# Kernel tuning notes

Measured on AMD Instinct MI355X. Metric: run time of the kernel, lower is better.

## Reference

```python
import jax, jax.numpy as jnp
import numpy as np

EPS = 1e-6
SCALE = 1.0
GRID_HEIGHT = 4.0
GRID_RES_Y = 1.0


def _perspective(mat, vec):
    # mat [3,4], vec [...,3] -> (points [...,2], flag [...,3])
    homog = jnp.einsum('ij,...j->...i', mat[:, :3], vec) + mat[:, 3]
    pos = homog[..., 2:3] > 0
    flag = jnp.concatenate([pos, pos, jnp.ones_like(pos)], axis=-1).astype(homog.dtype)
    homog = homog * flag  # zero x,y behind camera; z kept (flag[...,-1]=True)
    return homog[..., :2] / homog[..., 2:3], flag


def _fisheye(pts, k, D, flag):
    cx, cy, fx, fy = k[0, 2], k[1, 2], k[0, 0], k[1, 1]
    x = (pts[..., 0] - cx) / fx
    y = (pts[..., 1] - cy) / fy
    r = jnp.sqrt(x * x + y * y)
    th = jnp.arctan(r)
    t2 = th * th
    rad = th * (1 + D[0] * t2 + D[1] * t2 ** 2 + D[2] * t2 ** 3 + D[5] * t2 ** 4) / r
    xd = x * rad * fx + cx
    yd = y * rad * fy + cy
    return jnp.stack([xd, yd], axis=-1) * flag[..., :2]


def _pinhole(pts, k, D, flag):
    cx, cy, fx, fy = k[0, 2], k[1, 2], k[0, 0], k[1, 1]
    x = (pts[..., 0] - cx) / fx
    y = (pts[..., 1] - cy) / fy
    k1, k2, k3, p1, p2 = D[0], D[1], D[2], D[3], D[4]
    r2 = x * x + y * y
    poly = 1 + k1 * r2 + k2 * r2 * r2 + k3 * r2 * r2 * r2
    xd = x * poly + (2 * p1 * x * y + p2 * (r2 + 2 * x * x))
    yd = y * poly + (p1 * (r2 + 2 * y * y) + 2 * p2 * x * y)
    return jnp.stack([xd * fx + cx, yd * fy + cy], axis=-1) * flag[..., :2]


def _bilinear(img, coords):
    # torch F.grid_sample(align_corners=True, padding_mode='border'); img [C,H,W], coords [...,2] in [-1,1]
    C, H, W = img.shape
    x = jnp.clip((coords[..., 0] + 1) * 0.5 * (W - 1), 0.0, W - 1)
    y = jnp.clip((coords[..., 1] + 1) * 0.5 * (H - 1), 0.0, H - 1)
    x0 = jnp.floor(x)
    y0 = jnp.floor(y)
    wx = x - x0
    wy = y - y0
    x0i = x0.astype(jnp.int32)
    y0i = y0.astype(jnp.int32)
    x1i = jnp.minimum(x0i + 1, W - 1)
    y1i = jnp.minimum(y0i + 1, H - 1)
    flat = img.reshape(C, H * W)

    def g(yi, xi):
        return jnp.take(flat, (yi * W + xi).reshape(-1), axis=1).reshape((C,) + coords.shape[:-1])

    v00 = g(y0i, x0i)
    v01 = g(y0i, x1i)
    v10 = g(y1i, x0i)
    v11 = g(y1i, x1i)
    return v00 * (1 - wx) * (1 - wy) + v01 * wx * (1 - wy) + v10 * (1 - wx) * wy + v11 * wx * wy


def _per_image(feature, k, imu2c, post_rot, post_tran, undist, corner):
    C, Hf, Wf = feature.shape
    calib = k @ imu2c                                  # [3,4]
    pts, flag = _perspective(calib, corner)            # pts [Ny,Zd,Xd,2]
    pts = jnp.where(undist[-1] == 1,
                    _fisheye(pts, k, undist, flag),
                    _pinhole(pts, k, undist, flag))
    pts = jnp.einsum('ij,...j->...i', post_rot[:2, :2], pts) + post_tran[:2]
    nc = jnp.clip(2.0 * (pts / SCALE) - 1.0, -1.0, 1.0)  # [Ny,Zd,Xd,2]
    s0, s1 = slice(None, -1), slice(1, None)
    # 8 voxel corners -> [8, Ny-1, D, Wd, 2]
    corners8 = jnp.stack([nc[a, b, c] for a in (s0, s1) for b in (s0, s1) for c in (s0, s1)], axis=0)
    left = corners8[..., 0].min(0)
    right = corners8[..., 0].max(0)
    top = corners8[..., 1].min(0)
    bot = corners8[..., 1].max(0)
    Nh, D, Wd = left.shape
    bbox = jnp.stack([left, top, right, bot], axis=-1).reshape(Nh, D * Wd, 4)
    area = (bbox[..., 2] - bbox[..., 0]) * (bbox[..., 3] - bbox[..., 1]) * Hf * Wf * 0.25 + EPS  # [Nh,P]
    integ = jnp.cumsum(jnp.cumsum(feature, axis=-1), axis=-2)  # integral image [C,Hf,Wf]
    tl = _bilinear(integ, bbox[..., 0:2])
    br = _bilinear(integ, bbox[..., 2:4])
    tr = _bilinear(integ, jnp.stack([bbox[..., 2], bbox[..., 1]], axis=-1))
    bl = _bilinear(integ, jnp.stack([bbox[..., 0], bbox[..., 3]], axis=-1))
    vox = (tl + br - tr - bl) / area * (area > EPS)    # [C,Nh,P]
    return vox.reshape(C * Nh, D, Wd)                  # neck == '2d'


def _forward(features, ks, imu2cs, post_rots, post_trans, undists, grid):
    ys = -jnp.arange(0.0, GRID_HEIGHT, GRID_RES_Y) + GRID_HEIGHT / 2.0
    y_corners = jnp.stack([jnp.zeros_like(ys), ys, jnp.zeros_like(ys)], axis=-1)  # [Ny,3]
    corners = grid[:, None] + y_corners[None, :, None, None, :]                   # [B,Ny,Zd,Xd,3]
    per_cam = jax.vmap(_per_image, in_axes=(0, 0, 0, 0, 0, 0, None))

    def per_batch(f, k, m, pr, pt, ud, c):
        # drop_idx = [] -> all cameras kept; max over cameras
        return per_cam(f, k, m, pr, pt, ud, c).max(axis=0)

    return jax.vmap(per_batch)(features, ks, imu2cs, post_rots, post_trans, undists, corners)


def setup_inputs():
    key = jax.random.key(0)
    B, N, C, Hf, Wf = 1, 6, 64, 64, 176
    Zd = Xd = 129
    kf, ku = jax.random.split(key, 2)
    features = jax.random.normal(kf, (B, N, C, Hf, Wf), jnp.float32)
    # intrinsics (realistic pinhole values keep the projection numerically sane)
    K = np.zeros((B, N, 3, 3), np.float32)
    K[..., 0, 0] = 600.0
    K[..., 1, 1] = 600.0
    K[..., 0, 2] = 704.0
    K[..., 1, 2] = 256.0
    K[..., 2, 2] = 1.0
    ks = jnp.asarray(K)
    # extrinsics: per-camera yaw + small translation
    m = np.zeros((B, N, 3, 4), np.float32)
    for i in range(N):
        th = 0.25 * (i - 2.5)
        R = np.array([[np.cos(th), 0.0, np.sin(th)],
                      [0.0, 1.0, 0.0],
                      [-np.sin(th), 0.0, np.cos(th)]], np.float32)
        m[:, i, :, :3] = R
        m[:, i, :, 3] = np.array([0.1 * i, -1.5, 0.2], np.float32)
    imu2cs = jnp.asarray(m)
    pr = np.zeros((B, N, 3, 3), np.float32)
    pr[..., 0, 0] = 1.0 / 1408.0
    pr[..., 1, 1] = 1.0 / 512.0
    pr[..., 2, 2] = 1.0
    post_rots = jnp.asarray(pr)
    post_trans = jnp.zeros((B, N, 3), jnp.float32)
    und = 0.01 * np.array(jax.random.normal(ku, (B, N, 7)), np.float32)
    und[..., 6] = 0.0
    und[:, :3, 6] = 1.0  # first 3 cameras fisheye, rest pinhole
    undists = jnp.asarray(und)
    x = np.linspace(-40.0, 40.0, Xd, dtype=np.float32)
    z = np.linspace(3.0, 80.0, Zd, dtype=np.float32)
    zz, xx = np.meshgrid(z, x, indexing='ij')
    g = np.stack([xx, np.zeros_like(xx), zz], axis=-1)[None]  # [1,Zd,Xd,3]
    grid = jnp.asarray(np.broadcast_to(g, (B, Zd, Xd, 3)).copy())
    return {"features": features, "ks": ks, "imu2cs": imu2cs, "post_rots": post_rots,
            "post_trans": post_trans, "undists": undists, "grid": grid}


def reference(features, ks, imu2cs, post_rots, post_trans, undists, grid):
    return _forward(features, ks, imu2cs, post_rots, post_trans, undists, grid)
```

## Files before the change

### kernel.cpp

```cpp
#include <hip/hip_runtime.h>
#include <math.h>

#define NCAM 6
#define C_CH 64
#define HF   64
#define WF   176
#define GDIM 129
#define NY   4
#define NH   3
#define DD   128
#define WDIM 128
#define NP   (DD*WDIM)

#define ROWB (WF*C_CH*4)
#define COLB (C_CH*4)
#define IMGB ((size_t)HF*WF*C_CH*4)

struct alignas(16) BoxP {
    int   r0, r1, r2, r3;
    int   c0, c1, c2, c3;
    float wxL, wxR, wyT, wyB;
    float area;
    int   pad0, pad1, pad2;
};
static_assert(sizeof(BoxP) == 64, "BoxP size");

__device__ __forceinline__ int rfl_i(int x) {
    return __builtin_amdgcn_readfirstlane(x);
}
__device__ __forceinline__ float rfl_f(float x) {
    return __builtin_bit_cast(float, __builtin_amdgcn_readfirstlane(__builtin_bit_cast(int, x)));
}

__global__ __launch_bounds__(256) void k_rowcum(const float* __restrict__ feat,
                                                float* __restrict__ rowsum)
{
    __shared__ float T[WF * 65];
    __shared__ float S[4][C_CH];
    __shared__ float OFF[4][C_CH];
    const int h   = blockIdx.x;
    const int n   = blockIdx.y;
    const int tid = threadIdx.x;

    for (int idx = tid; idx < C_CH * WF; idx += 256) {
        const int cc = idx / WF;
        const int w  = idx % WF;
        T[w*65 + cc] = feat[((size_t)(n*C_CH + cc)*HF + h)*WF + w];
    }
    __syncthreads();
    {
        const int cc = tid & 63, seg = tid >> 6;
        const int w0 = seg * 44;
        float run = 0.0f;
        #pragma unroll
        for (int i = 0; i < 44; ++i) {
            run += T[(w0 + i)*65 + cc];
            T[(w0 + i)*65 + cc] = run;
        }
        S[seg][cc] = run;
    }
    __syncthreads();
    {
        const int cc = tid & 63, seg = tid >> 6;
        float off = 0.0f;
        #pragma unroll
        for (int s = 0; s < 3; ++s)
            if (s < seg) off += S[s][cc];
        OFF[seg][cc] = off;
    }
    __syncthreads();
    float* outp = rowsum + (size_t)(n*HF + h) * (WF * C_CH);
    for (int idx = tid; idx < WF * C_CH; idx += 256) {
        const int w  = idx >> 6;
        const int cc = idx & 63;
        outp[idx] = T[w*65 + cc] + OFF[w/44][cc];
    }
}

__global__ __launch_bounds__(256) void k_colcum(const float* __restrict__ rowsum,
                                                float* __restrict__ integ)
{
    __shared__ float tA[4][C_CH];
    const int x  = blockIdx.x;
    const int n  = blockIdx.y;
    const int c  = threadIdx.x & 63;
    const int hq = threadIdx.x >> 6;

    const float* base = rowsum + (size_t)n*HF*WF*C_CH + (size_t)x * C_CH + c;
    float e[16];
    #pragma unroll
    for (int i = 0; i < 16; ++i)
        e[i] = base[(size_t)(hq*16 + i) * (WF*C_CH)];
    #pragma unroll
    for (int i = 1; i < 16; ++i)
        e[i] += e[i-1];
    tA[hq][c] = e[15];
    __syncthreads();
    float off = 0.0f;
    #pragma unroll
    for (int s = 0; s < 3; ++s)
        if (s < hq) off += tA[s][c];
    float* outp = integ + (size_t)n*HF*WF*C_CH + (size_t)x * C_CH + c;
    #pragma unroll
    for (int i = 0; i < 16; ++i)
        outp[(size_t)(hq*16 + i) * (WF*C_CH)] = e[i] + off;
}

__global__ void k_boxproj(const float* __restrict__ ks,
                          const float* __restrict__ imu2cs,
                          const float* __restrict__ post_rots,
                          const float* __restrict__ post_trans,
                          const float* __restrict__ undists,
                          const float* __restrict__ grid,
                          BoxP* __restrict__ bp)
{
    const int idx = blockIdx.x * blockDim.x + threadIdx.x;
    if (idx >= NCAM * NH * NP) return;
    const int n  = idx / (NH * NP);
    const int r  = idx % (NH * NP);
    const int nh = r / NP;
    const int p  = r % NP;
    const int d  = p / WDIM;
    const int wd = p % WDIM;

    const float* k  = ks         + n * 9;
    const float* m  = imu2cs     + n * 12;
    const float* pr = post_rots  + n * 9;
    const float* pt = post_trans + n * 3;
    const float* D  = undists    + n * 7;

    float cal[12];
    #pragma unroll
    for (int i = 0; i < 3; ++i)
        #pragma unroll
        for (int j = 0; j < 4; ++j)
            cal[i*4+j] = k[i*3+0]*m[0*4+j] + k[i*3+1]*m[1*4+j] + k[i*3+2]*m[2*4+j];

    const float fx = k[0], fy = k[4], cx = k[2], cy = k[5];
    const bool fish = (D[6] == 1.0f);
    const float D0 = D[0], D1 = D[1], D2 = D[2], D3 = D[3], D4 = D[4], D5 = D[5];

    float left = 1e30f, right = -1e30f, top = 1e30f, bot = -1e30f;
    #pragma unroll
    for (int a = 0; a < 2; ++a) {
        const float vy = 2.0f - (float)(nh + a);
        #pragma unroll
        for (int b = 0; b < 2; ++b) {
            #pragma unroll
            for (int cc = 0; cc < 2; ++cc) {
                const int gz = d + b, gx = wd + cc;
                const float vx = grid[(gz*GDIM + gx)*3 + 0];
                const float vz = grid[(gz*GDIM + gx)*3 + 2];

                const float hx = cal[0]*vx + cal[1]*vy + cal[2]*vz  + cal[3];
                const float hy = cal[4]*vx + cal[5]*vy + cal[6]*vz  + cal[7];
                const float hz = cal[8]*vx + cal[9]*vy + cal[10]*vz + cal[11];

                const float fl = (hz > 0.0f) ? 1.0f : 0.0f;
                const float px = (hx * fl) / hz;
                const float py = (hy * fl) / hz;

                const float x = (px - cx) / fx;
                const float y = (py - cy) / fy;

                float xd, yd;
                if (fish) {
                    const float rr = sqrtf(x*x + y*y);
                    const float th = atanf(rr);
                    const float t2 = th * th;
                    const float t4 = t2 * t2;
                    const float rad = th * (1.0f + D0*t2 + D1*t4 + D2*(t2*t4) + D5*(t4*t4)) / rr;
                    xd = x * rad * fx + cx;
                    yd = y * rad * fy + cy;
                } else {
                    const float r2 = x*x + y*y;
                    const float poly = 1.0f + D0*r2 + D1*r2*r2 + D2*r2*r2*r2;
                    const float xdd = x*poly + (2.0f*D3*x*y + D4*(r2 + 2.0f*x*x));
                    const float ydd = y*poly + (D3*(r2 + 2.0f*y*y) + 2.0f*D4*x*y);
                    xd = xdd * fx + cx;
                    yd = ydd * fy + cy;
                }
                xd *= fl; yd *= fl;

                const float qx = pr[0]*xd + pr[1]*yd + pt[0];
                const float qy = pr[3]*xd + pr[4]*yd + pt[1];
                const float ncx = fminf(fmaxf(2.0f*qx - 1.0f, -1.0f), 1.0f);
                const float ncy = fminf(fmaxf(2.0f*qy - 1.0f, -1.0f), 1.0f);

                left  = fminf(left,  ncx);  right = fmaxf(right, ncx);
                top   = fminf(top,   ncy);  bot   = fmaxf(bot,   ncy);
            }
        }
    }

    const float area = (right - left) * (bot - top) * (float)HF * (float)WF * 0.25f + 1e-6f;

    const float xLp = fminf(fmaxf((left  + 1.0f) * 0.5f * (float)(WF-1), 0.0f), (float)(WF-1));
    const float xRp = fminf(fmaxf((right + 1.0f) * 0.5f * (float)(WF-1), 0.0f), (float)(WF-1));
    const float yTp = fminf(fmaxf((top   + 1.0f) * 0.5f * (float)(HF-1), 0.0f), (float)(HF-1));
    const float yBp = fminf(fmaxf((bot   + 1.0f) * 0.5f * (float)(HF-1), 0.0f), (float)(HF-1));
    const float xL0 = floorf(xLp), xR0 = floorf(xRp), yT0 = floorf(yTp), yB0 = floorf(yBp);

    const int ixL0 = (int)xL0, ixR0 = (int)xR0, iyT0 = (int)yT0, iyB0 = (int)yB0;
    const int ixL1 = min(ixL0 + 1, WF-1), ixR1 = min(ixR0 + 1, WF-1);
    const int iyT1 = min(iyT0 + 1, HF-1), iyB1 = min(iyB0 + 1, HF-1);

    BoxP o;
    o.r0 = iyT0 * ROWB; o.r1 = iyT1 * ROWB; o.r2 = iyB0 * ROWB; o.r3 = iyB1 * ROWB;
    o.c0 = ixL0 * COLB; o.c1 = ixL1 * COLB; o.c2 = ixR0 * COLB; o.c3 = ixR1 * COLB;
    o.wxL = xLp - xL0; o.wxR = xRp - xR0; o.wyT = yTp - yT0; o.wyB = yBp - yB0;
    o.area = area; o.pad0 = 0; o.pad1 = 0; o.pad2 = 0;
    bp[idx] = o;
}

__global__ __launch_bounds__(256) void k_sample(const float* __restrict__ integ,
                                                const BoxP* __restrict__ bp,
                                                float* __restrict__ out)
{
    __shared__ float sm[32][68];
    const int nh   = blockIdx.y;
    const int t    = blockIdx.x;
    const int d0   = (t >> 4) * 4;
    const int w0   = (t & 15) * 8;
    const int tid  = threadIdx.x;
    const int wave = __builtin_amdgcn_readfirstlane(tid >> 6);
    const int lane = tid & 63;
    const int g    = lane >> 4;
    const int q    = lane & 15;
    const int qoff = q * 16;
    const int d    = d0 + wave;

    auto ISSUE = [&](int cam, int pv,
                     float4& v0, float4& v1, float4& v2, float4& v3,
                     float& vg, float& wT, float& wB, float& ar) {
        const BoxP* bb = bp + ((cam*NH + nh)*NP + pv);
        ar = rfl_f(bb->area);
        const int r0 = rfl_i(bb->r0), r1 = rfl_i(bb->r1);
        const int r2 = rfl_i(bb->r2), r3 = rfl_i(bb->r3);
        const int c0 = rfl_i(bb->c0), c1 = rfl_i(bb->c1);
        const int c2 = rfl_i(bb->c2), c3 = rfl_i(bb->c3);
        const float wxL = rfl_f(bb->wxL), wxR = rfl_f(bb->wxR);
        wT = rfl_f(bb->wyT); wB = rfl_f(bb->wyB);
        const int co = (g == 0) ? c0 : (g == 1) ? c1 : (g == 2) ? c2 : c3;
        vg = (g == 0) ? (1.0f - wxL) : (g == 1) ? wxL
           : (g == 2) ? (wxR - 1.0f) : -wxR;
        const char* base = (const char*)integ + (size_t)cam * IMGB + (size_t)(co + qoff);
        v0 = *(const float4*)(base + r0);
        v1 = *(const float4*)(base + r1);
        v2 = *(const float4*)(base + r2);
        v3 = *(const float4*)(base + r3);
    };

    const int pbase = d * WDIM + w0;
    float4 a0, a1, a2, a3; float avg, awT, awB, aar;
    ISSUE(0, pbase, a0, a1, a2, a3, avg, awT, awB, aar);

    #pragma unroll 1
    for (int j = 0; j < 8; ++j) {
        const int pj = pbase + j;
        float4 vm = make_float4(-3.402823466e38f, -3.402823466e38f,
                                -3.402823466e38f, -3.402823466e38f);
        #pragma unroll
        for (int n = 0; n < NCAM; ++n) {
            float4 b0, b1, b2, b3; float bvg, bwT, bwB, bar;
            if (n < 5) {
                ISSUE(n+1, pj, b0, b1, b2, b3, bvg, bwT, bwB, bar);
            } else if (j < 7) {
                ISSUE(0, pj+1, b0, b1, b2, b3, bvg, bwT, bwB, bar);
            } else {
                b0 = a0; b1 = a1; b2 = a2; b3 = a3;
                bvg = avg; bwT = awT; bwB = awB; bar = aar;
            }
            const float u0 = 1.0f - awT, u1 = awT, u2 = awB - 1.0f, u3 = -awB;
            float px = fmaf(u0, a0.x, fmaf(u1, a1.x, fmaf(u2, a2.x, u3*a3.x))) * avg;
            float py = fmaf(u0, a0.y, fmaf(u1, a1.y, fmaf(u2, a2.y, u3*a3.y))) * avg;
            float pz = fmaf(u0, a0.z, fmaf(u1, a1.z, fmaf(u2, a2.z, u3*a3.z))) * avg;
            float pw = fmaf(u0, a0.w, fmaf(u1, a1.w, fmaf(u2, a2.w, u3*a3.w))) * avg;
            px += __shfl_xor(px, 16, 64); px += __shfl_xor(px, 32, 64);
            py += __shfl_xor(py, 16, 64); py += __shfl_xor(py, 32, 64);
            pz += __shfl_xor(pz, 16, 64); pz += __shfl_xor(pz, 32, 64);
            pw += __shfl_xor(pw, 16, 64); pw += __shfl_xor(pw, 32, 64);
            const float ia = __builtin_amdgcn_rcpf(aar);
            const bool ok = (aar > 1e-6f);
            vm.x = fmaxf(vm.x, ok ? px*ia : 0.0f);
            vm.y = fmaxf(vm.y, ok ? py*ia : 0.0f);
            vm.z = fmaxf(vm.z, ok ? pz*ia : 0.0f);
            vm.w = fmaxf(vm.w, ok ? pw*ia : 0.0f);
            a0 = b0; a1 = b1; a2 = b2; a3 = b3;
            avg = bvg; awT = bwT; awB = bwB; aar = bar;
        }
        if (g == 0) {
            *(float4*)&sm[wave*8 + j][4*q] = vm;
        }
    }
    __syncthreads();
    for (int idx = tid; idx < C_CH * 32; idx += 256) {
        const int jj = idx & 31;
        const int cc = idx >> 5;
        const int dd = d0 + (jj >> 3);
        const int ww = w0 + (jj & 7);
        out[(size_t)(cc*NH + nh)*NP + dd*WDIM + ww] = sm[jj][cc];
    }
}

extern "C" void kernel_launch(void* const* d_in, const int* in_sizes, int n_in,
                              void* d_out, int out_size, void* d_ws, size_t ws_size,
                              hipStream_t stream)
{
    const float* feats      = (const float*)d_in[0];
    const float* ks         = (const float*)d_in[1];
    const float* imu2cs     = (const float*)d_in[2];
    const float* post_rots  = (const float*)d_in[3];
    const float* post_trans = (const float*)d_in[4];
    const float* undists    = (const float*)d_in[5];
    const float* grid       = (const float*)d_in[6];
    float* out = (float*)d_out;

    char* ws = (char*)d_ws;
    size_t off = 0;
    float* rowsum = (float*)(ws + off);
    off += sizeof(float) * (size_t)NCAM * HF * WF * C_CH;
    off = (off + 255) & ~(size_t)255;
    float* integ = (float*)(ws + off);
    off += sizeof(float) * (size_t)NCAM * HF * WF * C_CH;
    off = (off + 255) & ~(size_t)255;
    BoxP* bp = (BoxP*)(ws + off);
    off += sizeof(BoxP) * (size_t)NCAM * NH * NP;
    (void)ws_size; (void)in_sizes; (void)n_in; (void)out_size;

    dim3 g1(HF, NCAM);
    k_rowcum<<<g1, 256, 0, stream>>>(feats, rowsum);

    dim3 g2(WF, NCAM);
    k_colcum<<<g2, 256, 0, stream>>>(rowsum, integ);

    dim3 g3((NCAM*NH*NP + 255)/256);
    k_boxproj<<<g3, 256, 0, stream>>>(ks, imu2cs, post_rots, post_trans, undists, grid, bp);

    dim3 g4(512, NH);
    k_sample<<<g4, 256, 0, stream>>>(integ, bp, out);
}
```

Before: 169.9 us.

## Restructure box sampling to thread-per-channel with compact camera-interleaved box params

The box-parameter buffer is reorganised so the six cameras of a voxel sit next to each other in a packed 32-byte record with byte-packed corner indices. The sample kernel now gives each lane one channel and has each wave handle 16 voxels. Each wave loads one voxel's parameters for all cameras into lanes, broadcasts them with readlane, prefetches the next voxel, and does the 16-tap bilinear integral-image lookup without cross-lane shuffles. The column-cumsum stage also now runs in place, which drops the separate rowsum buffer. The aim is to cut parameter-load traffic and shuffle overhead, at the cost of more scalar loads per lane (96 independent 4-byte gathers per voxel) and higher register pressure.

```diff
diff --git a/kernel.cpp b/kernel.cpp
--- a/kernel.cpp
+++ b/kernel.cpp
@@ -16,20 +16,9 @@
 #define COLB (C_CH*4)
 #define IMGB ((size_t)HF*WF*C_CH*4)
 
-struct alignas(16) BoxP {
-    int   r0, r1, r2, r3;
-    int   c0, c1, c2, c3;
-    float wxL, wxR, wyT, wyB;
-    float area;
-    int   pad0, pad1, pad2;
-};
-static_assert(sizeof(BoxP) == 64, "BoxP size");
-
-__device__ __forceinline__ int rfl_i(int x) {
-    return __builtin_amdgcn_readfirstlane(x);
-}
-__device__ __forceinline__ float rfl_f(float x) {
-    return __builtin_bit_cast(float, __builtin_amdgcn_readfirstlane(__builtin_bit_cast(int, x)));
+
+__device__ __forceinline__ float bcf(int x) {
+    return __builtin_bit_cast(float, x);
 }
 
 __global__ __launch_bounds__(256) void k_rowcum(const float* __restrict__ feat,
@@ -77,8 +66,7 @@
     }
 }
 
-__global__ __launch_bounds__(256) void k_colcum(const float* __restrict__ rowsum,
-                                                float* __restrict__ integ)
+__global__ __launch_bounds__(256) void k_colcum(float* __restrict__ integ)
 {
     __shared__ float tA[4][C_CH];
     const int x  = blockIdx.x;
@@ -86,7 +74,7 @@
     const int c  = threadIdx.x & 63;
     const int hq = threadIdx.x >> 6;
 
-    const float* base = rowsum + (size_t)n*HF*WF*C_CH + (size_t)x * C_CH + c;
+    float* base = integ + (size_t)n*HF*WF*C_CH + (size_t)x * C_CH + c;
     float e[16];
     #pragma unroll
     for (int i = 0; i < 16; ++i)
@@ -100,10 +88,9 @@
     #pragma unroll
     for (int s = 0; s < 3; ++s)
         if (s < hq) off += tA[s][c];
-    float* outp = integ + (size_t)n*HF*WF*C_CH + (size_t)x * C_CH + c;
     #pragma unroll
     for (int i = 0; i < 16; ++i)
-        outp[(size_t)(hq*16 + i) * (WF*C_CH)] = e[i] + off;
+        base[(size_t)(hq*16 + i) * (WF*C_CH)] = e[i] + off;
 }
 
 __global__ void k_boxproj(const float* __restrict__ ks,
@@ -112,16 +99,16 @@
                           const float* __restrict__ post_trans,
                           const float* __restrict__ undists,
                           const float* __restrict__ grid,
-                          BoxP* __restrict__ bp)
+                          int4* __restrict__ bp)
 {
     const int idx = blockIdx.x * blockDim.x + threadIdx.x;
     if (idx >= NCAM * NH * NP) return;
-    const int n  = idx / (NH * NP);
-    const int r  = idx % (NH * NP);
-    const int nh = r / NP;
-    const int p  = r % NP;
-    const int d  = p / WDIM;
-    const int wd = p % WDIM;
+    const int vox = idx / NCAM;
+    const int n   = idx - vox * NCAM;
+    const int nh  = vox / NP;
+    const int p   = vox - nh * NP;
+    const int d   = p / WDIM;
+    const int wd  = p - d * WDIM;
 
     const float* k  = ks         + n * 9;
     const float* m  = imu2cs     + n * 12;
@@ -201,105 +188,94 @@
     const float yBp = fminf(fmaxf((bot   + 1.0f) * 0.5f * (float)(HF-1), 0.0f), (float)(HF-1));
     const float xL0 = floorf(xLp), xR0 = floorf(xRp), yT0 = floorf(yTp), yB0 = floorf(yBp);
 
-    const int ixL0 = (int)xL0, ixR0 = (int)xR0, iyT0 = (int)yT0, iyB0 = (int)yB0;
-    const int ixL1 = min(ixL0 + 1, WF-1), ixR1 = min(ixR0 + 1, WF-1);
-    const int iyT1 = min(iyT0 + 1, HF-1), iyB1 = min(iyB0 + 1, HF-1);
-
-    BoxP o;
-    o.r0 = iyT0 * ROWB; o.r1 = iyT1 * ROWB; o.r2 = iyB0 * ROWB; o.r3 = iyB1 * ROWB;
-    o.c0 = ixL0 * COLB; o.c1 = ixL1 * COLB; o.c2 = ixR0 * COLB; o.c3 = ixR1 * COLB;
-    o.wxL = xLp - xL0; o.wxR = xRp - xR0; o.wyT = yTp - yT0; o.wyB = yBp - yB0;
-    o.area = area; o.pad0 = 0; o.pad1 = 0; o.pad2 = 0;
-    bp[idx] = o;
-}
-
-__global__ __launch_bounds__(256) void k_sample(const float* __restrict__ integ,
-                                                const BoxP* __restrict__ bp,
-                                                float* __restrict__ out)
-{
-    __shared__ float sm[32][68];
+    const int pyx = (int)yT0 | ((int)yB0 << 8) | ((int)xL0 << 16) | ((int)xR0 << 24);
+
+    int4 o0, o1;
+    o0.x = pyx;
+    o0.y = __builtin_bit_cast(int, xLp - xL0);
+    o0.z = __builtin_bit_cast(int, xRp - xR0);
+    o0.w = __builtin_bit_cast(int, yTp - yT0);
+    o1.x = __builtin_bit_cast(int, yBp - yB0);
+    o1.y = __builtin_bit_cast(int, area);
+    o1.z = 0; o1.w = 0;
+    bp[(size_t)idx*2 + 0] = o0;
+    bp[(size_t)idx*2 + 1] = o1;
+}
+
+__global__ __launch_bounds__(256, 4) void k_sample(const float* __restrict__ integ,
+                                                   const int* __restrict__ bpi,
+                                                   float* __restrict__ out)
+{
+    __shared__ float sm[64][65];
     const int nh   = blockIdx.y;
-    const int t    = blockIdx.x;
-    const int d0   = (t >> 4) * 4;
-    const int w0   = (t & 15) * 8;
+    const int p0   = blockIdx.x * 64;
     const int tid  = threadIdx.x;
     const int wave = __builtin_amdgcn_readfirstlane(tid >> 6);
-    const int lane = tid & 63;
-    const int g    = lane >> 4;
-    const int q    = lane & 15;
-    const int qoff = q * 16;
-    const int d    = d0 + wave;
-
-    auto ISSUE = [&](int cam, int pv,
-                     float4& v0, float4& v1, float4& v2, float4& v3,
-                     float& vg, float& wT, float& wB, float& ar) {
-        const BoxP* bb = bp + ((cam*NH + nh)*NP + pv);
-        ar = rfl_f(bb->area);
-        const int r0 = rfl_i(bb->r0), r1 = rfl_i(bb->r1);
-        const int r2 = rfl_i(bb->r2), r3 = rfl_i(bb->r3);
-        const int c0 = rfl_i(bb->c0), c1 = rfl_i(bb->c1);
-        const int c2 = rfl_i(bb->c2), c3 = rfl_i(bb->c3);
-        const float wxL = rfl_f(bb->wxL), wxR = rfl_f(bb->wxR);
-        wT = rfl_f(bb->wyT); wB = rfl_f(bb->wyB);
-        const int co = (g == 0) ? c0 : (g == 1) ? c1 : (g == 2) ? c2 : c3;
-        vg = (g == 0) ? (1.0f - wxL) : (g == 1) ? wxL
-           : (g == 2) ? (wxR - 1.0f) : -wxR;
-        const char* base = (const char*)integ + (size_t)cam * IMGB + (size_t)(co + qoff);
-        v0 = *(const float4*)(base + r0);
-        v1 = *(const float4*)(base + r1);
-        v2 = *(const float4*)(base + r2);
-        v3 = *(const float4*)(base + r3);
-    };
-
-    const int pbase = d * WDIM + w0;
-    float4 a0, a1, a2, a3; float avg, awT, awB, aar;
-    ISSUE(0, pbase, a0, a1, a2, a3, avg, awT, awB, aar);
-
+    const int c    = tid & 63;
+    const int pl   = (c < 48) ? c : (c - 48);
+
+    const int* bpw = bpi + (size_t)(nh*NP + p0 + wave*16) * 48;
+
+    int vpc = bpw[pl];
     #pragma unroll 1
-    for (int j = 0; j < 8; ++j) {
-        const int pj = pbase + j;
-        float4 vm = make_float4(-3.402823466e38f, -3.402823466e38f,
-                                -3.402823466e38f, -3.402823466e38f);
-        #pragma unroll
-        for (int n = 0; n < NCAM; ++n) {
-            float4 b0, b1, b2, b3; float bvg, bwT, bwB, bar;
-            if (n < 5) {
-                ISSUE(n+1, pj, b0, b1, b2, b3, bvg, bwT, bwB, bar);
-            } else if (j < 7) {
-                ISSUE(0, pj+1, b0, b1, b2, b3, bvg, bwT, bwB, bar);
-            } else {
-                b0 = a0; b1 = a1; b2 = a2; b3 = a3;
-                bvg = avg; bwT = awT; bwB = awB; bar = aar;
+    for (int j = 0; j < 16; ++j) {
+        int vpn = vpc;
+        if (j < 15) vpn = bpw[(j + 1) * 48 + pl];
+
+        float t[6][16];
+        float wxl[6], wxr[6], wyt[6], wyb[6], ar[6];
+        #pragma unroll
+        for (int cam = 0; cam < 6; ++cam) {
+            const int f0 = __builtin_amdgcn_readlane(vpc, cam*8 + 0);
+            wxl[cam] = bcf(__builtin_amdgcn_readlane(vpc, cam*8 + 1));
+            wxr[cam] = bcf(__builtin_amdgcn_readlane(vpc, cam*8 + 2));
+            wyt[cam] = bcf(__builtin_amdgcn_readlane(vpc, cam*8 + 3));
+            wyb[cam] = bcf(__builtin_amdgcn_readlane(vpc, cam*8 + 4));
+            ar[cam]  = bcf(__builtin_amdgcn_readlane(vpc, cam*8 + 5));
+            const int yT = f0 & 255, yB = (f0 >> 8) & 255;
+            const int xL = (f0 >> 16) & 255, xR = (f0 >> 24) & 255;
+            const int r0 = yT * ROWB, r2 = yB * ROWB;
+            const int c0 = xL * COLB, c2 = xR * COLB;
+            const char* b = (const char*)integ + (size_t)cam * IMGB;
+            #pragma unroll
+            for (int rr = 0; rr < 4; ++rr) {
+                const int ro = ((rr < 2) ? r0 : r2) + ((rr & 1) ? ROWB : 0);
+                #pragma unroll
+                for (int cc2 = 0; cc2 < 4; ++cc2) {
+                    const int co = ((cc2 < 2) ? c0 : c2) + ((cc2 & 1) ? COLB : 0);
+                    t[cam][rr*4 + cc2] = ((const float*)(b + (size_t)(ro + co)))[c];
+                }
             }
-            const float u0 = 1.0f - awT, u1 = awT, u2 = awB - 1.0f, u3 = -awB;
-            float px = fmaf(u0, a0.x, fmaf(u1, a1.x, fmaf(u2, a2.x, u3*a3.x))) * avg;
-            float py = fmaf(u0, a0.y, fmaf(u1, a1.y, fmaf(u2, a2.y, u3*a3.y))) * avg;
-            float pz = fmaf(u0, a0.z, fmaf(u1, a1.z, fmaf(u2, a2.z, u3*a3.z))) * avg;
-            float pw = fmaf(u0, a0.w, fmaf(u1, a1.w, fmaf(u2, a2.w, u3*a3.w))) * avg;
-            px += __shfl_xor(px, 16, 64); px += __shfl_xor(px, 32, 64);
-            py += __shfl_xor(py, 16, 64); py += __shfl_xor(py, 32, 64);
-            pz += __shfl_xor(pz, 16, 64); pz += __shfl_xor(pz, 32, 64);
-            pw += __shfl_xor(pw, 16, 64); pw += __shfl_xor(pw, 32, 64);
-            const float ia = __builtin_amdgcn_rcpf(aar);
-            const bool ok = (aar > 1e-6f);
-            vm.x = fmaxf(vm.x, ok ? px*ia : 0.0f);
-            vm.y = fmaxf(vm.y, ok ? py*ia : 0.0f);
-            vm.z = fmaxf(vm.z, ok ? pz*ia : 0.0f);
-            vm.w = fmaxf(vm.w, ok ? pw*ia : 0.0f);
-            a0 = b0; a1 = b1; a2 = b2; a3 = b3;
-            avg = bvg; awT = bwT; awB = bwB; aar = bar;
         }
-        if (g == 0) {
-            *(float4*)&sm[wave*8 + j][4*q] = vm;
+
+        float vmax = -3.402823466e38f;
+        #pragma unroll
+        for (int cam = 0; cam < 6; ++cam) {
+            const float A0 = fmaf(wxl[cam], t[cam][1]  - t[cam][0],  t[cam][0]);
+            const float B0 = fmaf(wxr[cam], t[cam][3]  - t[cam][2],  t[cam][2]);
+            const float A1 = fmaf(wxl[cam], t[cam][5]  - t[cam][4],  t[cam][4]);
+            const float B1 = fmaf(wxr[cam], t[cam][7]  - t[cam][6],  t[cam][6]);
+            const float A2 = fmaf(wxl[cam], t[cam][9]  - t[cam][8],  t[cam][8]);
+            const float B2 = fmaf(wxr[cam], t[cam][11] - t[cam][10], t[cam][10]);
+            const float A3 = fmaf(wxl[cam], t[cam][13] - t[cam][12], t[cam][12]);
+            const float B3 = fmaf(wxr[cam], t[cam][15] - t[cam][14], t[cam][14]);
+            const float d0 = A0 - B0, d1 = A1 - B1;
+            const float e0 = B2 - A2, e1 = B3 - A3;
+            const float s = fmaf(wyt[cam], d1 - d0, d0) + fmaf(wyb[cam], e1 - e0, e0);
+            float v = s * __builtin_amdgcn_rcpf(ar[cam]);
+            v = (ar[cam] > 1e-6f) ? v : 0.0f;
+            vmax = fmaxf(vmax, v);
         }
-    }
-    __syncthreads();
-    for (int idx = tid; idx < C_CH * 32; idx += 256) {
-        const int jj = idx & 31;
-        const int cc = idx >> 5;
-        const int dd = d0 + (jj >> 3);
-        const int ww = w0 + (jj & 7);
-        out[(size_t)(cc*NH + nh)*NP + dd*WDIM + ww] = sm[jj][cc];
+        sm[wave*16 + j][c] = vmax;
+        vpc = vpn;
+    }
+    __syncthreads();
+    #pragma unroll
+    for (int it = 0; it < 16; ++it) {
+        const int idx = it*256 + tid;
+        const int jj = idx & 63;
+        const int cc = idx >> 6;
+        out[(size_t)(cc*NH + nh)*NP + p0 + jj] = sm[jj][cc];
     }
 }
 
@@ -318,25 +294,22 @@
 
     char* ws = (char*)d_ws;
     size_t off = 0;
-    float* rowsum = (float*)(ws + off);
-    off += sizeof(float) * (size_t)NCAM * HF * WF * C_CH;
+    float* integ = (float*)(ws + off);
+    off += (size_t)NCAM * IMGB + 65536;
     off = (off + 255) & ~(size_t)255;
-    float* integ = (float*)(ws + off);
-    off += sizeof(float) * (size_t)NCAM * HF * WF * C_CH;
-    off = (off + 255) & ~(size_t)255;
-    BoxP* bp = (BoxP*)(ws + off);
-    off += sizeof(BoxP) * (size_t)NCAM * NH * NP;
+    int4* bp = (int4*)(ws + off);
+    off += (size_t)NCAM * NH * NP * 32 + 256;
     (void)ws_size; (void)in_sizes; (void)n_in; (void)out_size;
 
     dim3 g1(HF, NCAM);
-    k_rowcum<<<g1, 256, 0, stream>>>(feats, rowsum);
+    k_rowcum<<<g1, 256, 0, stream>>>(feats, integ);
 
     dim3 g2(WF, NCAM);
-    k_colcum<<<g2, 256, 0, stream>>>(rowsum, integ);
+    k_colcum<<<g2, 256, 0, stream>>>(integ);
 
     dim3 g3((NCAM*NH*NP + 255)/256);
     k_boxproj<<<g3, 256, 0, stream>>>(ks, imu2cs, post_rots, post_trans, undists, grid, bp);
 
-    dim3 g4(512, NH);
-    k_sample<<<g4, 256, 0, stream>>>(integ, bp, out);
-}
+    dim3 g4(NP/64, NH);
+    k_sample<<<g4, 256, 0, stream>>>(integ, (const int*)bp, out);
+}
```

Result: faster. 152.1 us (-10.5%).
